# Kernel optimization log

Hardware: AMD Instinct MI355X
Metric: run time of the kernel (lower is better)

The kernel has to match this reference:

```python
import jax, jax.numpy as jnp
import numpy as np

B, L, D, H, K = 4, 2048, 1024, 16, 3
HEAD_DIM = D // H
LN_EPS = 1e-5


def setup_inputs() -> dict:
    key = jax.random.key(0)
    ks = jax.random.split(key, 12)
    w = lambda k, shp: jax.random.normal(k, shp, jnp.float32) * (shp[-1] ** -0.5)
    return {
        "x": jax.random.normal(ks[0], (B, L, D), jnp.float32),
        "band_importance": jax.random.normal(ks[1], (1, L), jnp.float32) * 0.02,
        "Wq": w(ks[2], (D, D)), "bq": jnp.zeros((D,), jnp.float32),
        "Wk": w(ks[3], (D, D)), "bk": jnp.zeros((D,), jnp.float32),
        "Wv": w(ks[4], (D, D)), "bv": jnp.zeros((D,), jnp.float32),
        "Wo": w(ks[5], (D, D)), "bo": jnp.zeros((D,), jnp.float32),
        "gamma": jnp.ones((D,), jnp.float32),
        "beta": jnp.zeros((D,), jnp.float32),
    }


def reference(x, band_importance, Wq, bq, Wk, bk, Wv, bv, Wo, bo, gamma, beta):
    Bx, Lx, Dx = x.shape
    hd = Dx // H
    # top-k over softmax(band_importance); PyTorch bool attn_mask: True = BLOCKED
    imp = jax.nn.softmax(band_importance, axis=-1)[0]            # (L,)
    _, idx = jax.lax.top_k(imp, K)                               # (K,) int
    col_mask = jnp.zeros((Lx,), bool).at[idx].set(True)          # (L,) True -> masked out
    bias = jnp.where(col_mask, -jnp.inf, 0.0).astype(x.dtype)    # (L,)

    q = (x @ Wq.T + bq).reshape(Bx, Lx, H, hd)
    k_ = (x @ Wk.T + bk).reshape(Bx, Lx, H, hd)
    v = (x @ Wv.T + bv).reshape(Bx, Lx, H, hd)

    scale = 1.0 / np.sqrt(hd)
    scores = jnp.einsum("bqhd,bkhd->bhqk", q, k_) * scale + bias[None, None, None, :]
    attn = jax.nn.softmax(scores, axis=-1)                       # (B,H,L,L)
    ctx = jnp.einsum("bhqk,bkhd->bqhd", attn, v).reshape(Bx, Lx, Dx)
    attn_out = ctx @ Wo.T + bo

    y = x + attn_out                                             # residual
    mu = jnp.mean(y, axis=-1, keepdims=True)
    var = jnp.mean((y - mu) ** 2, axis=-1, keepdims=True)
    return (y - mu) * jax.lax.rsqrt(var + LN_EPS) * gamma + beta
```

## Files before the change

kernel.cpp:

```cpp
#include <hip/hip_runtime.h>

#define GAS __attribute__((address_space(1)))
#define LAS __attribute__((address_space(3)))

typedef __attribute__((ext_vector_type(8))) short short8;
typedef __attribute__((ext_vector_type(4))) float f32x4;
typedef __attribute__((ext_vector_type(16))) float f32x16;
typedef __attribute__((ext_vector_type(4))) unsigned int u32x4;

#define MFMA16(a,b,c) __builtin_amdgcn_mfma_f32_16x16x32_bf16(a,b,c,0,0,0)
#define MFMA32(a,b,c) __builtin_amdgcn_mfma_f32_32x32x16_bf16(a,b,c,0,0,0)

__device__ __forceinline__ unsigned short f2b(float f) {
  unsigned u = __float_as_uint(f);
  u += 0x7fffu + ((u >> 16) & 1u);
  return (unsigned short)(u >> 16);
}
__device__ __forceinline__ float b2f(unsigned short h) {
  return __uint_as_float(((unsigned)h) << 16);
}
__device__ __forceinline__ unsigned cvtpk(float a, float b) {
  unsigned r;
  asm("v_cvt_pk_bf16_f32 %0, %1, %2" : "=v"(r) : "v"(a), "v"(b));
  return r;
}
__device__ __forceinline__ void pl32swap(unsigned &x, unsigned &y) {
  auto r = __builtin_amdgcn_permlane32_swap((int)x, (int)y, false, false);
  x = (unsigned)r[0]; y = (unsigned)r[1];
}
__device__ __forceinline__ float xhalf_sum(float v) {
  auto r = __builtin_amdgcn_permlane32_swap(__float_as_int(v), __float_as_int(v), false, false);
  return __int_as_float(r[0]) + __int_as_float(r[1]);
}
__device__ __forceinline__ float fexp2(float x) {
  float r;
  asm("v_exp_f32 %0, %1" : "=v"(r) : "v"(x));
  return r;
}
__device__ __forceinline__ short8 ld8(const unsigned short* p) {
  return *reinterpret_cast<const short8*>(p);
}

union FW { u32x4 u; short8 s; };

__global__ void cvt_topk(const float* __restrict__ x,
                         const float* __restrict__ Wq, const float* __restrict__ Wk,
                         const float* __restrict__ Wv, const float* __restrict__ Wo,
                         const float* __restrict__ band,
                         unsigned short* __restrict__ xb,
                         unsigned short* __restrict__ Wqkvb,
                         unsigned short* __restrict__ Wob,
                         int* __restrict__ idxout) {
  const int bid = blockIdx.x;
  if (bid < 12288) {
    const float* src;
    unsigned short* dst;
    int idx;
    if (bid < 8192) {
      src = x; dst = xb; idx = bid * 256 + threadIdx.x;
    } else {
      int wb = bid - 8192;
      int seg = wb >> 10;
      idx = (wb & 1023) * 256 + threadIdx.x;
      src = (seg == 0) ? Wq : (seg == 1) ? Wk : (seg == 2) ? Wv : Wo;
      dst = (seg == 3) ? Wob : (Wqkvb + (size_t)seg * 1048576);
    }
    float4 v = reinterpret_cast<const float4*>(src)[idx];
    ushort4 o;
    o.x = f2b(v.x); o.y = f2b(v.y); o.z = f2b(v.z); o.w = f2b(v.w);
    reinterpret_cast<ushort4*>(dst)[idx] = o;
    return;
  }
  __shared__ float svals[256];
  __shared__ int   sidx[256];
  __shared__ int   chosen[3];
  const int t = threadIdx.x;
  for (int pass = 0; pass < 3; ++pass) {
    float best = -INFINITY; int bi = 1 << 30;
    for (int j = t; j < 2048; j += 256) {
      float v = band[j];
      bool skip = false;
      for (int p2 = 0; p2 < pass; ++p2) skip |= (chosen[p2] == j);
      if (!skip && (v > best || (v == best && j < bi))) { best = v; bi = j; }
    }
    svals[t] = best; sidx[t] = bi;
    __syncthreads();
    for (int s = 128; s > 0; s >>= 1) {
      if (t < s) {
        float v2 = svals[t + s]; int i2 = sidx[t + s];
        if (v2 > svals[t] || (v2 == svals[t] && i2 < sidx[t])) { svals[t] = v2; sidx[t] = i2; }
      }
      __syncthreads();
    }
    if (t == 0) chosen[pass] = sidx[0];
    __syncthreads();
  }
  if (t < 3) idxout[t] = chosen[t];
}

__global__ __launch_bounds__(512, 1) void gemm_qkv256(
    const unsigned short* __restrict__ A,
    const unsigned short* __restrict__ Wqkv,
    const float* __restrict__ bq, const float* __restrict__ bk,
    const float* __restrict__ bv,
    unsigned short* __restrict__ qout, unsigned short* __restrict__ kout,
    unsigned short* __restrict__ vtout, float qscale)
{
  __shared__ short Ls[3][2][8192];
  const int tid = threadIdx.x;
  const int w = tid >> 6, lane = tid & 63;
  const int wm = w >> 2, wn = w & 3;
  const int flat = blockIdx.y * 32 + blockIdx.x;
  const int swb = (flat & 7) * 48 + (flat >> 3);
  const int m0 = (swb & 31) * 256, n0 = (swb >> 5) * 256;

  const int seg = n0 >> 10;
  const float* biasp = (seg == 0) ? bq : (seg == 1) ? bk : bv;
  const float scale = (seg == 0) ? qscale : 1.0f;

  f32x4 acc[8][4];
  #pragma unroll
  for (int mt = 0; mt < 8; ++mt)
    #pragma unroll
    for (int nt = 0; nt < 4; ++nt)
      #pragma unroll
      for (int r = 0; r < 4; ++r) acc[mt][nt][r] = 0.f;

  const int srow = tid >> 2;
  const int scol = ((tid & 3) ^ ((srow >> 2) & 3)) * 8;
  const unsigned short* ap = A + (size_t)(m0 + srow) * 1024 + scol;
  const unsigned short* bp = Wqkv + (size_t)(n0 + srow) * 1024 + scol;
  const int ldst = tid * 8;

#define STG_A0(bufi, tt) __builtin_amdgcn_global_load_lds(                     \
    (const GAS void*)(ap + (size_t)(tt) * 32), (LAS void*)&Ls[bufi][0][ldst], 16, 0, 0)
#define STG_A1(bufi, tt) __builtin_amdgcn_global_load_lds(                     \
    (const GAS void*)(ap + (size_t)(tt) * 32 + 131072), (LAS void*)&Ls[bufi][0][4096 + ldst], 16, 0, 0)
#define STG_B0(bufi, tt) __builtin_amdgcn_global_load_lds(                     \
    (const GAS void*)(bp + (size_t)(tt) * 32), (LAS void*)&Ls[bufi][1][ldst], 16, 0, 0)
#define STG_B1(bufi, tt) __builtin_amdgcn_global_load_lds(                     \
    (const GAS void*)(bp + (size_t)(tt) * 32 + 131072), (LAS void*)&Ls[bufi][1][4096 + ldst], 16, 0, 0)

  const int r15 = lane & 15;
  const int fcol = ((lane >> 4) * 8) ^ (((r15 >> 2) & 3) << 3);
  const int arow0 = wm * 128 + r15;
  const int brow0 = wn * 64 + r15;

  STG_A0(0, 0); STG_A1(0, 0); STG_B0(0, 0); STG_B1(0, 0);
  STG_A0(1, 1); STG_A1(1, 1); STG_B0(1, 1); STG_B1(1, 1);

  for (int t = 0; t < 32; ++t) {
    if (t < 31) { asm volatile("s_waitcnt vmcnt(4)" ::: "memory"); }
    else        { asm volatile("s_waitcnt vmcnt(0)" ::: "memory"); }
    __builtin_amdgcn_sched_barrier(0);
    __builtin_amdgcn_s_barrier();
    __builtin_amdgcn_sched_barrier(0);
    const int buf = t % 3;
    const int sbuf = (t + 2) % 3;
    const short* Ab = &Ls[buf][0][0];
    const short* Bb = &Ls[buf][1][0];

    short8 bf[4];
    #pragma unroll
    for (int nt = 0; nt < 4; ++nt)
      bf[nt] = *reinterpret_cast<const short8*>(&Bb[(brow0 + nt * 16) * 32 + fcol]);

    #pragma unroll
    for (int ph = 0; ph < 4; ++ph) {
      if (t < 30) {
        if (ph == 0) STG_A0(sbuf, t + 2);
        else if (ph == 1) STG_A1(sbuf, t + 2);
        else if (ph == 2) STG_B0(sbuf, t + 2);
        else STG_B1(sbuf, t + 2);
      }
      short8 a0 = *reinterpret_cast<const short8*>(&Ab[(arow0 + (ph * 2) * 16) * 32 + fcol]);
      short8 a1 = *reinterpret_cast<const short8*>(&Ab[(arow0 + (ph * 2 + 1) * 16) * 32 + fcol]);
      __builtin_amdgcn_s_setprio(1);
      #pragma unroll
      for (int nt = 0; nt < 4; ++nt) {
        acc[ph * 2][nt] = MFMA16(a0, bf[nt], acc[ph * 2][nt]);
        acc[ph * 2 + 1][nt] = MFMA16(a1, bf[nt], acc[ph * 2 + 1][nt]);
      }
      __builtin_amdgcn_s_setprio(0);
    }

    asm volatile("s_waitcnt lgkmcnt(0)" ::: "memory");
    __builtin_amdgcn_sched_barrier(0);
  }

  if (seg == 2) {
    #pragma unroll
    for (int nt = 0; nt < 4; ++nt) {
      int coll = (n0 + wn * 64 + nt * 16 + r15) & 1023;
      float bval = biasp[coll];
      int h_ = coll >> 6, d_ = coll & 63;
      #pragma unroll
      for (int mt = 0; mt < 8; ++mt) {
        int rbase = m0 + wm * 128 + mt * 16 + ((lane >> 4) << 2);
        int b_ = rbase >> 11, lt_ = rbase & 2047;
        ushort4 pk;
        pk.x = f2b(acc[mt][nt][0] + bval);
        pk.y = f2b(acc[mt][nt][1] + bval);
        pk.z = f2b(acc[mt][nt][2] + bval);
        pk.w = f2b(acc[mt][nt][3] + bval);
        *reinterpret_cast<ushort4*>(
            &vtout[(((size_t)(b_ * 16 + h_)) * 64 + d_) * 2048 + lt_]) = pk;
      }
    }
  } else {
    unsigned short* outp = (seg == 0) ? qout : kout;
    #pragma unroll
    for (int nt = 0; nt < 4; ++nt) {
      int coll = (n0 + wn * 64 + nt * 16 + r15) & 1023;
      float bval = biasp[coll];
      int h_ = coll >> 6, d_ = coll & 63;
      #pragma unroll
      for (int mt = 0; mt < 8; ++mt) {
        int rbase = m0 + wm * 128 + mt * 16 + ((lane >> 4) << 2);
        #pragma unroll
        for (int r = 0; r < 4; ++r) {
          unsigned short val = f2b((acc[mt][nt][r] + bval) * scale);
          int row = rbase + r;
          int b_ = row >> 11, lt_ = row & 2047;
          outp[(((size_t)(b_ * 16 + h_)) * 2048 + lt_) * 64 + d_] = val;
        }
      }
    }
  }
}

__global__ __launch_bounds__(256) void gemm_wo(
    const unsigned short* __restrict__ A,
    const unsigned short* __restrict__ Bw,
    const float* __restrict__ bias,
    unsigned short* __restrict__ C)
{
  __shared__ short As[128][64];
  __shared__ short Bs[128][64];
  const int tid = threadIdx.x;
  const int w = tid >> 6, lane = tid & 63;
  const int wm = w >> 1, wn = w & 1;
  const int flat = blockIdx.y * 64 + blockIdx.x;
  const int swb = (flat & 7) * 64 + (flat >> 3);
  const int m0 = (swb & 63) * 128, n0 = (swb >> 6) * 128;
  const int rA = lane >> 3, cA = lane & 7;

  f32x4 acc[4][4];
  #pragma unroll
  for (int mt = 0; mt < 4; ++mt)
    #pragma unroll
    for (int nt = 0; nt < 4; ++nt)
      #pragma unroll
      for (int r = 0; r < 4; ++r) acc[mt][nt][r] = 0.f;

  for (int kt = 0; kt < 16; ++kt) {
    #pragma unroll
    for (int j = 0; j < 4; ++j) {
      int r = w * 32 + j * 8;
      const unsigned short* ga = A + (size_t)(m0 + r + rA) * 1024 + kt * 64 + cA * 8;
      __builtin_amdgcn_global_load_lds((const GAS void*)ga, (LAS void*)&As[r][0], 16, 0, 0);
      const unsigned short* gb = Bw + (size_t)(n0 + r + rA) * 1024 + kt * 64 + cA * 8;
      __builtin_amdgcn_global_load_lds((const GAS void*)gb, (LAS void*)&Bs[r][0], 16, 0, 0);
    }
    __syncthreads();
    #pragma unroll
    for (int kc = 0; kc < 2; ++kc) {
      short8 a[4], b[4];
      #pragma unroll
      for (int mt = 0; mt < 4; ++mt)
        a[mt] = *reinterpret_cast<const short8*>(
            &As[wm * 64 + mt * 16 + (lane & 15)][kc * 32 + (lane >> 4) * 8]);
      #pragma unroll
      for (int nt = 0; nt < 4; ++nt)
        b[nt] = *reinterpret_cast<const short8*>(
            &Bs[wn * 64 + nt * 16 + (lane & 15)][kc * 32 + (lane >> 4) * 8]);
      __builtin_amdgcn_s_setprio(1);
      #pragma unroll
      for (int mt = 0; mt < 4; ++mt)
        #pragma unroll
        for (int nt = 0; nt < 4; ++nt)
          acc[mt][nt] = MFMA16(a[mt], b[nt], acc[mt][nt]);
      __builtin_amdgcn_s_setprio(0);
    }
    __syncthreads();
  }
  #pragma unroll
  for (int nt = 0; nt < 4; ++nt) {
    int col = n0 + wn * 64 + nt * 16 + (lane & 15);
    float bval = bias[col];
    #pragma unroll
    for (int mt = 0; mt < 4; ++mt) {
      int rbase = m0 + wm * 64 + mt * 16 + ((lane >> 4) << 2);
      #pragma unroll
      for (int r = 0; r < 4; ++r)
        C[(size_t)(rbase + r) * 1024 + col] = f2b(acc[mt][nt][r] + bval);
    }
  }
}

#define PACK8(S, j0, OUT) {                                        \
    unsigned A_ = cvtpk(S[(j0)+0], S[(j0)+1]);                     \
    unsigned B_ = cvtpk(S[(j0)+4], S[(j0)+5]);                     \
    unsigned C_ = cvtpk(S[(j0)+2], S[(j0)+3]);                     \
    unsigned D_ = cvtpk(S[(j0)+6], S[(j0)+7]);                     \
    pl32swap(A_, B_); pl32swap(C_, D_);                            \
    FW f_; f_.u[0] = A_; f_.u[1] = C_; f_.u[2] = B_; f_.u[3] = D_; \
    OUT = f_.s; }

__global__ __launch_bounds__(512, 2) void attn8(
    const unsigned short* __restrict__ qg,
    const unsigned short* __restrict__ kg,
    const unsigned short* __restrict__ vtg,
    const int* __restrict__ midx,
    unsigned short* __restrict__ ctx)
{
  __shared__ short Ks[2][64 * 64];
  __shared__ short Vs[2][64 * 64];
  const int tid = threadIdx.x, w = tid >> 6, lane = tid & 63;
  const int flat = blockIdx.y * 8 + blockIdx.x;
  const int swzb = (flat & 7) * 64 + (flat >> 3);
  const int qt = swzb & 7, bh = swzb >> 3;
  const int q0 = qt * 256;
  const int lo5 = lane & 31, hi = lane >> 5;
  const int i0 = midx[0], i1 = midx[1], i2 = midx[2];

  const int qrow = q0 + w * 32 + lo5;
  const unsigned short* qp = qg + ((size_t)bh * 2048 + qrow) * 64 + hi * 8;
  short8 qf[4];
  #pragma unroll
  for (int ds = 0; ds < 4; ++ds) qf[ds] = ld8(qp + ds * 16);

  f32x16 oacc0, oacc1, lacc;
  #pragma unroll
  for (int r = 0; r < 16; ++r) { oacc0[r] = 0.f; oacc1[r] = 0.f; lacc[r] = 0.f; }

  const int srow = tid >> 3;
  const int swzoff = (((tid & 7) ^ (srow & 7))) * 8;
  const unsigned short* kp = kg + ((size_t)bh * 2048 + srow) * 64 + swzoff;
  const unsigned short* vp = vtg + ((size_t)bh * 64 + srow) * 2048 + swzoff;

#define STAGE8(bufi, tt) do {                                                  \
    __builtin_amdgcn_global_load_lds((const GAS void*)(kp + (size_t)(tt) * 4096), \
        (LAS void*)&Ks[bufi][w * 512], 16, 0, 0);                              \
    __builtin_amdgcn_global_load_lds((const GAS void*)(vp + (tt) * 64),        \
        (LAS void*)&Vs[bufi][w * 512], 16, 0, 0);                              \
  } while (0)

  STAGE8(0, 0);
  STAGE8(1, 1);

  for (int t = 0; t < 32; ++t) {
    const int buf = t & 1;
    if (t < 31) { asm volatile("s_waitcnt vmcnt(2)" ::: "memory"); }
    else        { asm volatile("s_waitcnt vmcnt(0)" ::: "memory"); }
    __builtin_amdgcn_sched_barrier(0);
    __builtin_amdgcn_s_barrier();
    __builtin_amdgcn_sched_barrier(0);

    short8 kf[8];
    #pragma unroll
    for (int ds = 0; ds < 4; ++ds) {
      int cw = ds * 2 + hi;
      kf[2 * ds] = *reinterpret_cast<const short8*>(
          &Ks[buf][lo5 * 64 + ((cw ^ (lo5 & 7)) * 8)]);
      kf[2 * ds + 1] = *reinterpret_cast<const short8*>(
          &Ks[buf][(32 + lo5) * 64 + ((cw ^ (lo5 & 7)) * 8)]);
    }

    f32x16 s0, s1;
    #pragma unroll
    for (int r = 0; r < 16; ++r) { s0[r] = 0.f; s1[r] = 0.f; }
    __builtin_amdgcn_s_setprio(1);
    #pragma unroll
    for (int ds = 0; ds < 4; ++ds) {
      s0 = MFMA32(kf[2 * ds], qf[ds], s0);
      s1 = MFMA32(kf[2 * ds + 1], qf[ds], s1);
    }
    __builtin_amdgcn_s_setprio(0);

    short8 vf[8];
    #pragma unroll
    for (int ks = 0; ks < 4; ++ks) {
      int cw = ks * 2 + hi;
      vf[2 * ks] = *reinterpret_cast<const short8*>(
          &Vs[buf][lo5 * 64 + ((cw ^ (lo5 & 7)) * 8)]);
      vf[2 * ks + 1] = *reinterpret_cast<const short8*>(
          &Vs[buf][(32 + lo5) * 64 + ((cw ^ (lo5 & 7)) * 8)]);
    }

    #pragma unroll
    for (int r = 0; r < 16; ++r) s0[r] = fexp2(s0[r]);
    #pragma unroll
    for (int r = 0; r < 16; ++r) s1[r] = fexp2(s1[r]);

    int t64 = t * 64;
    bool tm = ((unsigned)(i0 - t64) < 64u) | ((unsigned)(i1 - t64) < 64u) |
              ((unsigned)(i2 - t64) < 64u);
    if (tm) {
      #pragma unroll
      for (int r = 0; r < 16; ++r) {
        int kg0 = t64 + (r & 3) + 8 * (r >> 2) + 4 * hi;
        int kg1 = kg0 + 32;
        if (kg0 == i0 || kg0 == i1 || kg0 == i2) s0[r] = 0.f;
        if (kg1 == i0 || kg1 == i1 || kg1 == i2) s1[r] = 0.f;
      }
    }

    #pragma unroll
    for (int r = 0; r < 16; ++r) lacc[r] += s0[r] + s1[r];

    short8 pa[4];
    PACK8(s0, 0, pa[0]); PACK8(s0, 8, pa[1]);
    PACK8(s1, 0, pa[2]); PACK8(s1, 8, pa[3]);

    asm volatile("s_waitcnt lgkmcnt(0)" ::: "memory");
    __builtin_amdgcn_sched_barrier(0);
    __builtin_amdgcn_s_barrier();
    __builtin_amdgcn_sched_barrier(0);
    if (t < 30) STAGE8(buf, t + 2);

    __builtin_amdgcn_s_setprio(1);
    #pragma unroll
    for (int ks = 0; ks < 4; ++ks) {
      oacc0 = MFMA32(pa[ks], vf[2 * ks], oacc0);
      oacc1 = MFMA32(pa[ks], vf[2 * ks + 1], oacc1);
    }
    __builtin_amdgcn_s_setprio(0);
  }

  float lsum = 0.f;
  #pragma unroll
  for (int r = 0; r < 16; ++r) lsum += lacc[r];
  lsum = xhalf_sum(lsum);
  const int bb = bh >> 4, hh = bh & 15;
  float rinv = 1.0f / lsum;
  #pragma unroll
  for (int r = 0; r < 16; ++r) {
    int row = (r & 3) + 8 * (r >> 2) + 4 * hi;
    float rv = __int_as_float(__builtin_amdgcn_ds_bpermute(
        (row + (lane & 32)) * 4, __float_as_int(rinv)));
    int qr = q0 + w * 32 + row;
    size_t base = (((size_t)(bb * 2048 + qr)) * 16 + hh) * 64;
    ctx[base + lo5]      = f2b(oacc0[r] * rv);
    ctx[base + 32 + lo5] = f2b(oacc1[r] * rv);
  }
}

__global__ __launch_bounds__(256) void resid_ln(
    const float* __restrict__ x, const unsigned short* __restrict__ ao,
    const float* __restrict__ gamma, const float* __restrict__ beta,
    float* __restrict__ out)
{
  const int row = blockIdx.x, t = threadIdx.x;
  const size_t base = (size_t)row * 1024;
  float4 xv = reinterpret_cast<const float4*>(x + base)[t];
  ushort4 av = reinterpret_cast<const ushort4*>(ao + base)[t];
  float y[4] = {xv.x + b2f(av.x), xv.y + b2f(av.y), xv.z + b2f(av.z), xv.w + b2f(av.w)};
  float sum = y[0] + y[1] + y[2] + y[3];
  float sq = y[0] * y[0] + y[1] * y[1] + y[2] * y[2] + y[3] * y[3];
  #pragma unroll
  for (int off = 1; off < 64; off <<= 1) {
    sum += __shfl_xor(sum, off);
    sq += __shfl_xor(sq, off);
  }
  __shared__ float s1[4], s2[4];
  int w = t >> 6, lane = t & 63;
  if (lane == 0) { s1[w] = sum; s2[w] = sq; }
  __syncthreads();
  sum = s1[0] + s1[1] + s1[2] + s1[3];
  sq = s2[0] + s2[1] + s2[2] + s2[3];
  float mu = sum * (1.f / 1024.f);
  float var = sq * (1.f / 1024.f) - mu * mu;
  float inv = rsqrtf(var + 1e-5f);
  float4 gv = reinterpret_cast<const float4*>(gamma)[t];
  float4 bv = reinterpret_cast<const float4*>(beta)[t];
  float4 o;
  o.x = (y[0] - mu) * inv * gv.x + bv.x;
  o.y = (y[1] - mu) * inv * gv.y + bv.y;
  o.z = (y[2] - mu) * inv * gv.z + bv.z;
  o.w = (y[3] - mu) * inv * gv.w + bv.w;
  reinterpret_cast<float4*>(out + base)[t] = o;
}

extern "C" void kernel_launch(void* const* d_in, const int* in_sizes, int n_in,
                              void* d_out, int out_size, void* d_ws, size_t ws_size,
                              hipStream_t stream)
{
  const float* x     = (const float*)d_in[0];
  const float* band  = (const float*)d_in[1];
  const float* Wq    = (const float*)d_in[2];
  const float* bq    = (const float*)d_in[3];
  const float* Wk    = (const float*)d_in[4];
  const float* bk    = (const float*)d_in[5];
  const float* Wv    = (const float*)d_in[6];
  const float* bv    = (const float*)d_in[7];
  const float* Wo    = (const float*)d_in[8];
  const float* bo    = (const float*)d_in[9];
  const float* gamma = (const float*)d_in[10];
  const float* beta  = (const float*)d_in[11];
  float* out = (float*)d_out;

  char* ws = (char*)d_ws;
  int*            idxw  = (int*)(ws);
  unsigned short* xb    = (unsigned short*)(ws + 4096);
  unsigned short* Wqkvb = (unsigned short*)(ws + 16781312);
  unsigned short* Wob   = (unsigned short*)(ws + 23072768);
  unsigned short* qb    = (unsigned short*)(ws + 25169920);
  unsigned short* kb    = (unsigned short*)(ws + 41947136);
  unsigned short* ctxb  = (unsigned short*)(ws + 58724352);
  unsigned short* vtb   = (unsigned short*)(ws + 75501568);
  unsigned short* aob   = qb;

  const float QSCALE = 0.125f * 1.44269504f;

  cvt_topk<<<12289, 256, 0, stream>>>(x, Wq, Wk, Wv, Wo, band, xb, Wqkvb, Wob, idxw);

  gemm_qkv256<<<dim3(32, 12), 512, 0, stream>>>(xb, Wqkvb, bq, bk, bv,
                                                qb, kb, vtb, QSCALE);

  attn8<<<dim3(8, 64), 512, 0, stream>>>(qb, kb, vtb, idxw, ctxb);

  gemm_wo<<<dim3(64, 8), 256, 0, stream>>>(ctxb, Wob, bo, aob);

  resid_ln<<<8192, 256, 0, stream>>>(x, aob, gamma, beta, out);
}
```

Baseline: 225.9 us.

## Process two 32-row query tiles per wave to reuse K/V tiles

Each wave in the attention kernel now handles 64 query rows as two 32-row sub-tiles, so every block covers 512 queries and the grid is halved. Each staged K/V tile in shared memory is reused across twice as many query rows, which halves global K/V traffic and barrier overhead per unit of work. The PV MFMAs for the two sub-tiles are interleaved. Costs: more accumulator registers and launch bounds dropped to one block per CU, giving lower occupancy and only 256 blocks, which may leave CUs underfilled.

```diff
diff --git a/kernel.cpp b/kernel.cpp
--- a/kernel.cpp
+++ b/kernel.cpp
@@ -307,7 +307,7 @@
     FW f_; f_.u[0] = A_; f_.u[1] = C_; f_.u[2] = B_; f_.u[3] = D_; \
     OUT = f_.s; }
 
-__global__ __launch_bounds__(512, 2) void attn8(
+__global__ __launch_bounds__(512, 1) void attn9(
     const unsigned short* __restrict__ qg,
     const unsigned short* __restrict__ kg,
     const unsigned short* __restrict__ vtg,
@@ -317,37 +317,46 @@
   __shared__ short Ks[2][64 * 64];
   __shared__ short Vs[2][64 * 64];
   const int tid = threadIdx.x, w = tid >> 6, lane = tid & 63;
-  const int flat = blockIdx.y * 8 + blockIdx.x;
-  const int swzb = (flat & 7) * 64 + (flat >> 3);
-  const int qt = swzb & 7, bh = swzb >> 3;
-  const int q0 = qt * 256;
+  const int flat = blockIdx.y * 4 + blockIdx.x;
+  const int swzb = (flat & 7) * 32 + (flat >> 3);
+  const int qt = swzb & 3, bh = swzb >> 2;
+  const int q0 = qt * 512;
   const int lo5 = lane & 31, hi = lane >> 5;
   const int i0 = midx[0], i1 = midx[1], i2 = midx[2];
 
-  const int qrow = q0 + w * 32 + lo5;
-  const unsigned short* qp = qg + ((size_t)bh * 2048 + qrow) * 64 + hi * 8;
-  short8 qf[4];
-  #pragma unroll
-  for (int ds = 0; ds < 4; ++ds) qf[ds] = ld8(qp + ds * 16);
-
-  f32x16 oacc0, oacc1, lacc;
-  #pragma unroll
-  for (int r = 0; r < 16; ++r) { oacc0[r] = 0.f; oacc1[r] = 0.f; lacc[r] = 0.f; }
+  const int qra = q0 + w * 64 + lo5;
+  const unsigned short* qpa = qg + ((size_t)bh * 2048 + qra) * 64 + hi * 8;
+  const unsigned short* qpb = qpa + (size_t)32 * 64;
+  short8 qfa[4], qfb[4];
+  #pragma unroll
+  for (int ds = 0; ds < 4; ++ds) {
+    qfa[ds] = ld8(qpa + ds * 16);
+    qfb[ds] = ld8(qpb + ds * 16);
+  }
+
+  f32x16 oacc0a, oacc1a, oacc0b, oacc1b;
+  f32x4 lacca, laccb;
+  #pragma unroll
+  for (int r = 0; r < 16; ++r) {
+    oacc0a[r] = 0.f; oacc1a[r] = 0.f; oacc0b[r] = 0.f; oacc1b[r] = 0.f;
+  }
+  #pragma unroll
+  for (int r = 0; r < 4; ++r) { lacca[r] = 0.f; laccb[r] = 0.f; }
 
   const int srow = tid >> 3;
   const int swzoff = (((tid & 7) ^ (srow & 7))) * 8;
   const unsigned short* kp = kg + ((size_t)bh * 2048 + srow) * 64 + swzoff;
   const unsigned short* vp = vtg + ((size_t)bh * 64 + srow) * 2048 + swzoff;
 
-#define STAGE8(bufi, tt) do {                                                  \
+#define STAGE9(bufi, tt) do {                                                  \
     __builtin_amdgcn_global_load_lds((const GAS void*)(kp + (size_t)(tt) * 4096), \
         (LAS void*)&Ks[bufi][w * 512], 16, 0, 0);                              \
     __builtin_amdgcn_global_load_lds((const GAS void*)(vp + (tt) * 64),        \
         (LAS void*)&Vs[bufi][w * 512], 16, 0, 0);                              \
   } while (0)
 
-  STAGE8(0, 0);
-  STAGE8(1, 1);
+  STAGE9(0, 0);
+  STAGE9(1, 1);
 
   for (int t = 0; t < 32; ++t) {
     const int buf = t & 1;
@@ -367,14 +376,48 @@
           &Ks[buf][(32 + lo5) * 64 + ((cw ^ (lo5 & 7)) * 8)]);
     }
 
+    const int t64 = t * 64;
+    const bool tm = ((unsigned)(i0 - t64) < 64u) | ((unsigned)(i1 - t64) < 64u) |
+                    ((unsigned)(i2 - t64) < 64u);
+
     f32x16 s0, s1;
     #pragma unroll
     for (int r = 0; r < 16; ++r) { s0[r] = 0.f; s1[r] = 0.f; }
     __builtin_amdgcn_s_setprio(1);
     #pragma unroll
     for (int ds = 0; ds < 4; ++ds) {
-      s0 = MFMA32(kf[2 * ds], qf[ds], s0);
-      s1 = MFMA32(kf[2 * ds + 1], qf[ds], s1);
+      s0 = MFMA32(kf[2 * ds], qfa[ds], s0);
+      s1 = MFMA32(kf[2 * ds + 1], qfa[ds], s1);
+    }
+    __builtin_amdgcn_s_setprio(0);
+
+    #pragma unroll
+    for (int r = 0; r < 16; ++r) s0[r] = fexp2(s0[r]);
+    #pragma unroll
+    for (int r = 0; r < 16; ++r) s1[r] = fexp2(s1[r]);
+    if (tm) {
+      #pragma unroll
+      for (int r = 0; r < 16; ++r) {
+        int kg0 = t64 + (r & 3) + 8 * (r >> 2) + 4 * hi;
+        int kg1 = kg0 + 32;
+        if (kg0 == i0 || kg0 == i1 || kg0 == i2) s0[r] = 0.f;
+        if (kg1 == i0 || kg1 == i1 || kg1 == i2) s1[r] = 0.f;
+      }
+    }
+    #pragma unroll
+    for (int r = 0; r < 16; ++r) lacca[r & 3] += s0[r] + s1[r];
+
+    short8 paa0, paa1, paa2, paa3;
+    PACK8(s0, 0, paa0); PACK8(s0, 8, paa1);
+    PACK8(s1, 0, paa2); PACK8(s1, 8, paa3);
+
+    #pragma unroll
+    for (int r = 0; r < 16; ++r) { s0[r] = 0.f; s1[r] = 0.f; }
+    __builtin_amdgcn_s_setprio(1);
+    #pragma unroll
+    for (int ds = 0; ds < 4; ++ds) {
+      s0 = MFMA32(kf[2 * ds], qfb[ds], s0);
+      s1 = MFMA32(kf[2 * ds + 1], qfb[ds], s1);
     }
     __builtin_amdgcn_s_setprio(0);
 
@@ -392,10 +435,6 @@
     for (int r = 0; r < 16; ++r) s0[r] = fexp2(s0[r]);
     #pragma unroll
     for (int r = 0; r < 16; ++r) s1[r] = fexp2(s1[r]);
-
-    int t64 = t * 64;
-    bool tm = ((unsigned)(i0 - t64) < 64u) | ((unsigned)(i1 - t64) < 64u) |
-              ((unsigned)(i2 - t64) < 64u);
     if (tm) {
       #pragma unroll
       for (int r = 0; r < 16; ++r) {
@@ -405,44 +444,50 @@
         if (kg1 == i0 || kg1 == i1 || kg1 == i2) s1[r] = 0.f;
       }
     }
-
-    #pragma unroll
-    for (int r = 0; r < 16; ++r) lacc[r] += s0[r] + s1[r];
-
-    short8 pa[4];
-    PACK8(s0, 0, pa[0]); PACK8(s0, 8, pa[1]);
-    PACK8(s1, 0, pa[2]); PACK8(s1, 8, pa[3]);
+    #pragma unroll
+    for (int r = 0; r < 16; ++r) laccb[r & 3] += s0[r] + s1[r];
+
+    short8 pab0, pab1, pab2, pab3;
+    PACK8(s0, 0, pab0); PACK8(s0, 8, pab1);
+    PACK8(s1, 0, pab2); PACK8(s1, 8, pab3);
 
     asm volatile("s_waitcnt lgkmcnt(0)" ::: "memory");
     __builtin_amdgcn_sched_barrier(0);
     __builtin_amdgcn_s_barrier();
     __builtin_amdgcn_sched_barrier(0);
-    if (t < 30) STAGE8(buf, t + 2);
+    if (t < 30) STAGE9(buf, t + 2);
 
     __builtin_amdgcn_s_setprio(1);
-    #pragma unroll
-    for (int ks = 0; ks < 4; ++ks) {
-      oacc0 = MFMA32(pa[ks], vf[2 * ks], oacc0);
-      oacc1 = MFMA32(pa[ks], vf[2 * ks + 1], oacc1);
-    }
+    oacc0a = MFMA32(paa0, vf[0], oacc0a); oacc1a = MFMA32(paa0, vf[1], oacc1a);
+    oacc0b = MFMA32(pab0, vf[0], oacc0b); oacc1b = MFMA32(pab0, vf[1], oacc1b);
+    oacc0a = MFMA32(paa1, vf[2], oacc0a); oacc1a = MFMA32(paa1, vf[3], oacc1a);
+    oacc0b = MFMA32(pab1, vf[2], oacc0b); oacc1b = MFMA32(pab1, vf[3], oacc1b);
+    oacc0a = MFMA32(paa2, vf[4], oacc0a); oacc1a = MFMA32(paa2, vf[5], oacc1a);
+    oacc0b = MFMA32(pab2, vf[4], oacc0b); oacc1b = MFMA32(pab2, vf[5], oacc1b);
+    oacc0a = MFMA32(paa3, vf[6], oacc0a); oacc1a = MFMA32(paa3, vf[7], oacc1a);
+    oacc0b = MFMA32(pab3, vf[6], oacc0b); oacc1b = MFMA32(pab3, vf[7], oacc1b);
     __builtin_amdgcn_s_setprio(0);
   }
 
-  float lsum = 0.f;
-  #pragma unroll
-  for (int r = 0; r < 16; ++r) lsum += lacc[r];
-  lsum = xhalf_sum(lsum);
+  float lsa = lacca[0] + lacca[1] + lacca[2] + lacca[3];
+  float lsb = laccb[0] + laccb[1] + laccb[2] + laccb[3];
+  lsa = xhalf_sum(lsa);
+  lsb = xhalf_sum(lsb);
   const int bb = bh >> 4, hh = bh & 15;
-  float rinv = 1.0f / lsum;
+  float rinva = 1.0f / lsa, rinvb = 1.0f / lsb;
   #pragma unroll
   for (int r = 0; r < 16; ++r) {
     int row = (r & 3) + 8 * (r >> 2) + 4 * hi;
-    float rv = __int_as_float(__builtin_amdgcn_ds_bpermute(
-        (row + (lane & 32)) * 4, __float_as_int(rinv)));
-    int qr = q0 + w * 32 + row;
-    size_t base = (((size_t)(bb * 2048 + qr)) * 16 + hh) * 64;
-    ctx[base + lo5]      = f2b(oacc0[r] * rv);
-    ctx[base + 32 + lo5] = f2b(oacc1[r] * rv);
+    int addr = (row + (lane & 32)) * 4;
+    float rva = __int_as_float(__builtin_amdgcn_ds_bpermute(addr, __float_as_int(rinva)));
+    float rvb = __int_as_float(__builtin_amdgcn_ds_bpermute(addr, __float_as_int(rinvb)));
+    int qr = q0 + w * 64 + row;
+    size_t basea = (((size_t)(bb * 2048 + qr)) * 16 + hh) * 64;
+    size_t baseb = (((size_t)(bb * 2048 + qr + 32)) * 16 + hh) * 64;
+    ctx[basea + lo5]      = f2b(oacc0a[r] * rva);
+    ctx[basea + 32 + lo5] = f2b(oacc1a[r] * rva);
+    ctx[baseb + lo5]      = f2b(oacc0b[r] * rvb);
+    ctx[baseb + 32 + lo5] = f2b(oacc1b[r] * rvb);
   }
 }
 
@@ -518,7 +563,7 @@
   gemm_qkv256<<<dim3(32, 12), 512, 0, stream>>>(xb, Wqkvb, bq, bk, bv,
                                                 qb, kb, vtb, QSCALE);
 
-  attn8<<<dim3(8, 64), 512, 0, stream>>>(qb, kb, vtb, idxw, ctxb);
+  attn9<<<dim3(4, 64), 512, 0, stream>>>(qb, kb, vtb, idxw, ctxb);
 
   gemm_wo<<<dim3(64, 8), 256, 0, stream>>>(ctxb, Wob, bo, aob);
 
```

Result: slower. 255.6 us (+13.1%).
